# Kernel tuning notes

Hardware: AMD Instinct MI355X
Metric: run time of the kernel (lower is better)

## Reference

```python
import jax, jax.numpy as jnp
import numpy as np

N = 100000          # nodes
E = 3200000         # edges (avg degree 32)
F_IN = 128          # num_features
HID = 128           # hidden_channels
C = 8               # num_classes
G = 64              # graphs in batch
EPS = 1e-5


def setup_inputs() -> dict:
    key = jax.random.key(0)
    ks = jax.random.split(key, 10)
    x = jax.random.normal(ks[0], (N, F_IN), dtype=jnp.float32)
    edge_index = jax.random.randint(ks[1], (2, E), 0, N, dtype=jnp.int64)
    batch = jnp.sort(jax.random.randint(ks[2], (N,), 0, G, dtype=jnp.int64))
    # parameters
    glorot1 = float(np.sqrt(6.0 / (F_IN + HID)))
    W1 = jax.random.uniform(ks[3], (F_IN, HID), minval=-glorot1, maxval=glorot1, dtype=jnp.float32)
    conv1_bias = jnp.zeros((HID,), jnp.float32)
    bn_weight = jnp.ones((F_IN,), jnp.float32)
    bn_bias = jnp.zeros((F_IN,), jnp.float32)
    ln_weight = jnp.ones((HID,), jnp.float32)
    ln_bias = jnp.zeros((HID,), jnp.float32)
    glorot2 = float(np.sqrt(6.0 / (HID + C)))
    lin_W = jax.random.uniform(ks[4], (C, HID), minval=-glorot2, maxval=glorot2, dtype=jnp.float32)
    lin_b = jnp.zeros((C,), jnp.float32)
    return {"x": x, "edge_index": edge_index, "batch": batch,
            "bn_weight": bn_weight, "bn_bias": bn_bias,
            "W1": W1, "conv1_bias": conv1_bias,
            "ln_weight": ln_weight, "ln_bias": ln_bias,
            "lin_W": lin_W, "lin_b": lin_b}


def reference(x, edge_index, batch, bn_weight, bn_bias, W1, conv1_bias,
              ln_weight, ln_bias, lin_W, lin_b):
    n = x.shape[0]
    # BatchNorm1d over nodes (training-mode batch statistics, biased var)
    mu = x.mean(axis=0)
    var = x.var(axis=0)
    x = (x - mu) * jax.lax.rsqrt(var + EPS) * bn_weight + bn_bias
    # GCNConv: linear transform, add self-loops, symmetric normalization, scatter-add
    h = x @ W1                                   # [N, HID]
    loops = jnp.arange(n, dtype=edge_index.dtype)
    row = jnp.concatenate([edge_index[0], loops])  # source nodes
    col = jnp.concatenate([edge_index[1], loops])  # target nodes
    deg = jax.ops.segment_sum(jnp.ones_like(col, dtype=h.dtype), col, num_segments=N)
    dinv = jax.lax.rsqrt(deg)                    # deg >= 1 due to self-loops
    norm = dinv[row] * dinv[col]                 # [E+N]
    msg = h[row] * norm[:, None]                 # gather + scale
    h = jax.ops.segment_sum(msg, col, num_segments=N) + conv1_bias
    h = jax.nn.relu(h)
    # PyG LayerNorm, mode='graph', batch=None: normalize over the whole tensor
    h = h - h.mean()
    h = h * jax.lax.rsqrt(h.var() + EPS)
    h = h * ln_weight + ln_bias
    # global mean pool per graph
    counts = jax.ops.segment_sum(jnp.ones((n,), h.dtype), batch, num_segments=G)
    sums = jax.ops.segment_sum(h, batch, num_segments=G)
    g = sums / jnp.maximum(counts, 1.0)[:, None]  # [G, HID]
    return g @ lin_W.T + lin_b                    # [G, C]
```

## Files before the change

kernel.cpp:

```cpp
#include <hip/hip_runtime.h>

#define NN 100000
#define NE 3200000
#define F 128
#define NG 64
#define NC 8
#define EPSF 1e-5f

#define AGG_BLOCKS 25000
#define LDSTRIDE 136
#define BN_BLOCKS 1024

#define NBK 256
#define BNODES 391
#define BCAP 14336
#define CHUNK 4096
#define P1_BLOCKS ((NE + CHUNK - 1) / CHUNK)

typedef __attribute__((ext_vector_type(8))) short bf16x8;
typedef __attribute__((ext_vector_type(4))) float f32x4;
typedef _Float16 f16x2 __attribute__((ext_vector_type(2)));

union U32H2 { unsigned int u; f16x2 h; };
__device__ __forceinline__ f16x2 asH2(unsigned int u) { U32H2 c; c.u = u; return c.h; }
__device__ __forceinline__ unsigned int asU32(f16x2 h) { U32H2 c; c.h = h; return c.u; }

__device__ __forceinline__ unsigned short f2bf(float f) {
    unsigned int u = __float_as_uint(f);
    u = u + 0x7FFFu + ((u >> 16) & 1u);
    return (unsigned short)(u >> 16);
}
__device__ __forceinline__ unsigned short f2h_bits(float f) {
    union { _Float16 h; unsigned short u; } c;
    c.h = (_Float16)f;
    return c.u;
}

__global__ void bn_partial_k(const float* __restrict__ x, float* __restrict__ part,
                             int n, int rpb) {
    int tid = threadIdx.x, col = tid & 127, half = tid >> 7;
    int r0 = blockIdx.x * rpb, r1 = min(n, r0 + rpb);
    float s = 0.f, ss = 0.f;
    for (int r = r0 + half; r < r1; r += 2) {
        float v = x[(size_t)r * F + col];
        s += v; ss += v * v;
    }
    __shared__ float sh[512];
    sh[tid] = s; sh[256 + tid] = ss;
    __syncthreads();
    if (half == 0) {
        part[blockIdx.x * 256 + col]       = sh[col] + sh[col + 128];
        part[blockIdx.x * 256 + 128 + col] = sh[256 + col] + sh[256 + col + 128];
    }
}

__global__ void bn_finalize_k(const float* __restrict__ part,
                              const float* __restrict__ bnw, const float* __restrict__ bnb,
                              float* __restrict__ scale, float* __restrict__ shift, int n) {
    int col = blockIdx.x, tid = threadIdx.x;
    float s = 0.f, ss = 0.f;
    #pragma unroll
    for (int i = 0; i < 4; ++i) {
        int b = tid + i * 256;
        s  += part[b * 256 + col];
        ss += part[b * 256 + 128 + col];
    }
    __shared__ float shs[256], shss[256];
    shs[tid] = s; shss[tid] = ss;
    __syncthreads();
    for (int o = 128; o > 0; o >>= 1) {
        if (tid < o) { shs[tid] += shs[tid + o]; shss[tid] += shss[tid + o]; }
        __syncthreads();
    }
    if (tid == 0) {
        float mu  = shs[0] / (float)n;
        float var = shss[0] / (float)n - mu * mu;
        float rstd = rsqrtf(var + EPSF);
        float sc = bnw[col] * rstd;
        scale[col] = sc;
        shift[col] = bnb[col] - mu * sc;
    }
}

__global__ void prep_both_k(const float* __restrict__ W1, const float* __restrict__ scale,
                            const float* __restrict__ shift,
                            unsigned short* __restrict__ WpT, float* __restrict__ S) {
    int b = blockIdx.x, tid = threadIdx.x;
    if (b < 64) {
        int idx = b * 256 + tid;
        int k = idx >> 7, j = idx & 127;
        WpT[j * F + k] = f2bf(scale[k] * W1[idx]);
    } else {
        int j = b - 64;
        __shared__ float sh[256];
        sh[tid] = (tid < 128) ? shift[tid] * W1[tid * F + j] : 0.f;
        __syncthreads();
        for (int o = 128; o > 0; o >>= 1) {
            if (tid < o) sh[tid] += sh[tid + o];
            __syncthreads();
        }
        if (tid == 0) S[j] = sh[0];
    }
}

__global__ __launch_bounds__(256) void bucket_k(const int* __restrict__ ei,
                                                int* __restrict__ bcur,
                                                unsigned int* __restrict__ bbuf) {
    __shared__ int cntl[NBK];
    __shared__ int basel[NBK];
    __shared__ int gbase[NBK];
    __shared__ unsigned int ent[CHUNK];
    __shared__ unsigned char bid[CHUNK];
    int tid = threadIdx.x;
    int e0 = blockIdx.x * CHUNK;
    int ecnt = min(NE - e0, CHUNK);
    cntl[tid] = 0;
    __syncthreads();
    int myr[16], myc[16], myl[16];
    #pragma unroll
    for (int k = 0; k < 16; ++k) {
        int i = tid + k * 256;
        if (i < ecnt) {
            int r = ei[e0 + i];
            int c = ei[NE + e0 + i];
            myr[k] = r; myc[k] = c;
            myl[k] = atomicAdd(&cntl[(unsigned)c / BNODES], 1);
        } else { myr[k] = -1; myc[k] = 0; myl[k] = 0; }
    }
    __syncthreads();
    int myv = cntl[tid];
    basel[tid] = myv;
    __syncthreads();
    for (int o = 1; o < 256; o <<= 1) {
        int t = (tid >= o) ? basel[tid - o] : 0;
        __syncthreads();
        basel[tid] += t;
        __syncthreads();
    }
    basel[tid] -= myv;
    gbase[tid] = atomicAdd(&bcur[tid], myv);
    __syncthreads();
    #pragma unroll
    for (int k = 0; k < 16; ++k) {
        if (myr[k] >= 0) {
            int b = (unsigned)myc[k] / BNODES;
            int s = basel[b] + myl[k];
            ent[s] = ((unsigned)myr[k] << 9) | (unsigned)(myc[k] - b * BNODES);
            bid[s] = (unsigned char)b;
        }
    }
    __syncthreads();
    for (int s = tid; s < ecnt; s += 256) {
        unsigned int v = ent[s];
        int b = bid[s];
        int idx = s - basel[b] + gbase[b];
        if (idx < BCAP) bbuf[(size_t)b * BCAP + idx] = v;
    }
}

__global__ void bbase_k(const int* __restrict__ bcur, int* __restrict__ bbase,
                        int* __restrict__ offs) {
    int tid = threadIdx.x;
    __shared__ int s[256];
    int v = bcur[tid];
    s[tid] = v;
    __syncthreads();
    for (int o = 1; o < 256; o <<= 1) {
        int t = (tid >= o) ? s[tid - o] : 0;
        __syncthreads();
        s[tid] += t;
        __syncthreads();
    }
    bbase[tid] = s[tid] - v;
    if (tid == 255) offs[NN] = s[255];
}

__global__ void csr_k(const unsigned int* __restrict__ bbuf, const int* __restrict__ bcur,
                      const int* __restrict__ bbase,
                      int* __restrict__ offs, float* __restrict__ dinv,
                      int* __restrict__ srow) {
    int b = blockIdx.x, tid = threadIdx.x;
    __shared__ int h0[512], hA[512], hB[512];
    h0[tid] = 0; h0[tid + 256] = 0;
    __syncthreads();
    int m = min(bcur[b], BCAP);
    for (int i = tid; i < m; i += 256)
        atomicAdd(&h0[bbuf[(size_t)b * BCAP + i] & 511u], 1);
    __syncthreads();
    hA[tid] = h0[tid]; hA[tid + 256] = h0[tid + 256];
    __syncthreads();
    int* src = hA; int* dst = hB;
    for (int o = 1; o < 512; o <<= 1) {
        int i0 = tid, i1 = tid + 256;
        dst[i0] = src[i0] + ((i0 >= o) ? src[i0 - o] : 0);
        dst[i1] = src[i1] + ((i1 >= o) ? src[i1 - o] : 0);
        __syncthreads();
        int* tmp = src; src = dst; dst = tmp;
    }
    int nbase = b * BNODES;
    int base = bbase[b];
    int lim = min(BNODES, NN - nbase);
    for (int i = tid; i < lim; i += 256) {
        int d = h0[i];
        offs[nbase + i] = base + src[i] - d;
        dinv[nbase + i] = rsqrtf((float)d + 1.0f);
    }
    dst[tid] = src[tid] - h0[tid];
    dst[tid + 256] = src[tid + 256] - h0[tid + 256];
    __syncthreads();
    for (int i = tid; i < m; i += 256) {
        unsigned int v = bbuf[(size_t)b * BCAP + i];
        int dstl = (int)(v & 511u);
        int pos = base + atomicAdd(&dst[dstl], 1);
        srow[pos] = (int)(v >> 9);
    }
}

__global__ __launch_bounds__(256) void gemm_k(const float* __restrict__ x,
                                              const unsigned short* __restrict__ WpT,
                                              const float* __restrict__ S,
                                              const float* __restrict__ dinv,
                                              unsigned short* __restrict__ hf, int n) {
    __shared__ unsigned short wt[128 * LDSTRIDE];
    __shared__ unsigned short xt[64 * LDSTRIDE];
    int tid = threadIdx.x;
    int row0 = blockIdx.x * 64;
    for (int i = tid; i < 2048; i += 256) {
        int r = i >> 4, c = (i & 15) * 8;
        uint4 v = *(const uint4*)&WpT[r * F + c];
        *(uint4*)&wt[r * LDSTRIDE + c] = v;
    }
    for (int i = tid; i < 2048; i += 256) {
        int r = i >> 5, c = (i & 31) * 4;
        float4 v = make_float4(0.f, 0.f, 0.f, 0.f);
        if (row0 + r < n) v = *(const float4*)&x[(size_t)(row0 + r) * F + c];
        unsigned int p0 = (unsigned int)f2bf(v.x) | ((unsigned int)f2bf(v.y) << 16);
        unsigned int p1 = (unsigned int)f2bf(v.z) | ((unsigned int)f2bf(v.w) << 16);
        *(uint2*)&xt[r * LDSTRIDE + c] = make_uint2(p0, p1);
    }
    __syncthreads();
    int wv = tid >> 6, lane = tid & 63;
    int lm = lane & 15, lk = lane >> 4;
    bf16x8 afrag[4];
    #pragma unroll
    for (int kk = 0; kk < 4; ++kk)
        afrag[kk] = *(bf16x8*)&xt[(wv * 16 + lm) * LDSTRIDE + kk * 32 + lk * 8];
    float dv[4];
    #pragma unroll
    for (int j = 0; j < 4; ++j) {
        int r = row0 + wv * 16 + lk * 4 + j;
        dv[j] = (r < n) ? dinv[r] : 1.0f;
    }
    #pragma unroll
    for (int nt = 0; nt < 8; ++nt) {
        float sv = S[nt * 16 + lm];
        f32x4 acc = {sv, sv, sv, sv};
        #pragma unroll
        for (int kk = 0; kk < 4; ++kk) {
            bf16x8 b = *(bf16x8*)&wt[(nt * 16 + lm) * LDSTRIDE + kk * 32 + lk * 8];
            acc = __builtin_amdgcn_mfma_f32_16x16x32_bf16(afrag[kk], b, acc, 0, 0, 0);
        }
        #pragma unroll
        for (int j = 0; j < 4; ++j) {
            int r = row0 + wv * 16 + lk * 4 + j;
            if (r < n) hf[(size_t)r * F + nt * 16 + lm] = f2h_bits(acc[j] * dv[j]);
        }
    }
}

__global__ __launch_bounds__(256) void agg_k(const uint4* __restrict__ hb4,
                                             const int* __restrict__ srow,
                                             const int* __restrict__ offs,
                                             const float* __restrict__ dinv,
                                             const float* __restrict__ bias,
                                             uint4* __restrict__ h2p4,
                                             float* __restrict__ lnpart, int n) {
    int lane = threadIdx.x & 63, wv = threadIdx.x >> 6;
    int node = blockIdx.x * 4 + wv;
    int cg = lane & 15;
    int sub = lane >> 4;
    float s_part = 0.f, ss_part = 0.f;
    if (node < n) {
        int st = offs[node], en = offs[node + 1];
        float di = dinv[node];
        f16x2 a0 = {0.f16, 0.f16}, a1 = a0, a2 = a0, a3 = a0;
        if (sub == 0) {
            uint4 qs = hb4[(size_t)node * 16 + cg];
            a0 += asH2(qs.x); a1 += asH2(qs.y); a2 += asH2(qs.z); a3 += asH2(qs.w);
        }
        const uint4 qz = make_uint4(0u, 0u, 0u, 0u);
        for (int base = st; base < en; base += 64) {
            int m = en - base; if (m > 64) m = 64;
            int sv = (lane < m) ? srow[base + lane] : 0;
            int nq = (m + 3) >> 2;
            int k = 0;
            for (; k + 2 <= nq; k += 2) {
                int i0 = 4 * k + sub, i1 = i0 + 4;
                int sr0 = __shfl(sv, i0), sr1 = __shfl(sv, i1);
                bool v0 = i0 < m, v1 = i1 < m;
                uint4 q0 = hb4[(size_t)(v0 ? sr0 : node) * 16 + cg];
                uint4 q1 = hb4[(size_t)(v1 ? sr1 : node) * 16 + cg];
                if (!v0) q0 = qz;
                if (!v1) q1 = qz;
                a0 += asH2(q0.x); a1 += asH2(q0.y); a2 += asH2(q0.z); a3 += asH2(q0.w);
                a0 += asH2(q1.x); a1 += asH2(q1.y); a2 += asH2(q1.z); a3 += asH2(q1.w);
            }
            for (; k < nq; ++k) {
                int i0 = 4 * k + sub;
                int sr0 = __shfl(sv, i0);
                bool v0 = i0 < m;
                uint4 q0 = hb4[(size_t)(v0 ? sr0 : node) * 16 + cg];
                if (!v0) q0 = qz;
                a0 += asH2(q0.x); a1 += asH2(q0.y); a2 += asH2(q0.z); a3 += asH2(q0.w);
            }
        }
        a0 += asH2((unsigned int)__shfl_xor((int)asU32(a0), 16));
        a1 += asH2((unsigned int)__shfl_xor((int)asU32(a1), 16));
        a2 += asH2((unsigned int)__shfl_xor((int)asU32(a2), 16));
        a3 += asH2((unsigned int)__shfl_xor((int)asU32(a3), 16));
        a0 += asH2((unsigned int)__shfl_xor((int)asU32(a0), 32));
        a1 += asH2((unsigned int)__shfl_xor((int)asU32(a1), 32));
        a2 += asH2((unsigned int)__shfl_xor((int)asU32(a2), 32));
        a3 += asH2((unsigned int)__shfl_xor((int)asU32(a3), 32));
        float acc[8] = {(float)a0[0], (float)a0[1], (float)a1[0], (float)a1[1],
                        (float)a2[0], (float)a2[1], (float)a3[0], (float)a3[1]};
        float4 b0 = *(const float4*)&bias[cg * 8];
        float4 b1 = *(const float4*)&bias[cg * 8 + 4];
        float bv[8] = {b0.x, b0.y, b0.z, b0.w, b1.x, b1.y, b1.z, b1.w};
        float r[8];
        #pragma unroll
        for (int j = 0; j < 8; ++j) r[j] = fmaxf(fmaf(acc[j], di, bv[j]), 0.f);
        if (sub == 0) {
            uint4 p;
            p.x = asU32(f16x2{(_Float16)r[0], (_Float16)r[1]});
            p.y = asU32(f16x2{(_Float16)r[2], (_Float16)r[3]});
            p.z = asU32(f16x2{(_Float16)r[4], (_Float16)r[5]});
            p.w = asU32(f16x2{(_Float16)r[6], (_Float16)r[7]});
            h2p4[(size_t)node * 16 + cg] = p;
            #pragma unroll
            for (int j = 0; j < 8; ++j) {
                s_part += r[j];
                ss_part += r[j] * r[j];
            }
        }
    }
    __shared__ float sh[512];
    sh[threadIdx.x] = s_part; sh[256 + threadIdx.x] = ss_part;
    __syncthreads();
    for (int o = 128; o > 0; o >>= 1) {
        if (threadIdx.x < o) {
            sh[threadIdx.x] += sh[threadIdx.x + o];
            sh[256 + threadIdx.x] += sh[256 + threadIdx.x + o];
        }
        __syncthreads();
    }
    if (threadIdx.x == 0) {
        lnpart[blockIdx.x * 2]     = sh[0];
        lnpart[blockIdx.x * 2 + 1] = sh[256];
    }
}

__global__ void pool1_k(const unsigned int* __restrict__ h2p, const int* __restrict__ batch,
                        float* __restrict__ gsum, int n) {
    int tid = threadIdx.x, cp = tid & 63, half = tid >> 6;
    int n0 = blockIdx.x * 256, n1 = min(n, n0 + 256);
    int r = n0 + half;
    if (r >= n1) return;
    int gcur = batch[r];
    float a0 = 0.f, a1 = 0.f;
    for (; r < n1; r += 4) {
        int g = batch[r];
        f16x2 hp = asH2(h2p[(size_t)r * 64 + cp]);
        if (g != gcur) {
            atomicAdd(&gsum[gcur * F + cp * 2], a0);
            atomicAdd(&gsum[gcur * F + cp * 2 + 1], a1);
            a0 = a1 = 0.f; gcur = g;
        }
        a0 += (float)hp[0];
        a1 += (float)hp[1];
    }
    atomicAdd(&gsum[gcur * F + cp * 2], a0);
    atomicAdd(&gsum[gcur * F + cp * 2 + 1], a1);
}

__global__ void pool2_k(const float* __restrict__ gsum, const int* __restrict__ batch,
                        const float* __restrict__ lnpart, int nb,
                        const float* __restrict__ lnw, const float* __restrict__ lnb,
                        const float* __restrict__ linW, const float* __restrict__ linb,
                        float* __restrict__ out, int n) {
    int g = blockIdx.x, tid = threadIdx.x;
    __shared__ double shd[512];
    __shared__ float lnmu, lnrs;
    double s = 0.0, ss = 0.0;
    for (int i = tid; i < nb; i += 256) {
        s  += (double)lnpart[2 * i];
        ss += (double)lnpart[2 * i + 1];
    }
    shd[tid] = s; shd[256 + tid] = ss;
    __syncthreads();
    for (int o = 128; o > 0; o >>= 1) {
        if (tid < o) { shd[tid] += shd[tid + o]; shd[256 + tid] += shd[256 + tid + o]; }
        __syncthreads();
    }
    __shared__ int bounds[2];
    if (tid == 0) {
        double cnt = (double)NN * (double)F;
        double mu = shd[0] / cnt;
        double var = shd[256] / cnt - mu * mu;
        lnmu = (float)mu;
        lnrs = (float)(1.0 / sqrt(var + (double)EPSF));
    }
    if (tid < 2) {
        int target = g + tid;
        int lo = 0, hi = n;
        while (lo < hi) {
            int mid = (lo + hi) >> 1;
            if (batch[mid] < target) lo = mid + 1; else hi = mid;
        }
        bounds[tid] = lo;
    }
    __syncthreads();
    int cg = bounds[1] - bounds[0];
    __shared__ float vals[128];
    if (tid < 128) {
        float v = 0.f;
        if (cg > 0) {
            float m = gsum[g * F + tid] / (float)cg;
            v = (m - lnmu) * lnrs * lnw[tid] + lnb[tid];
        }
        vals[tid] = v;
    }
    __syncthreads();
    if (tid < NC) {
        float o = linb[tid];
        for (int k = 0; k < F; ++k) o = fmaf(vals[k], linW[tid * F + k], o);
        out[g * NC + tid] = o;
    }
}

extern "C" void kernel_launch(void* const* d_in, const int* in_sizes, int n_in,
                              void* d_out, int out_size, void* d_ws, size_t ws_size,
                              hipStream_t stream) {
    const float* x     = (const float*)d_in[0];
    const int*   ei    = (const int*)d_in[1];
    const int*   batch = (const int*)d_in[2];
    const float* bnw   = (const float*)d_in[3];
    const float* bnb   = (const float*)d_in[4];
    const float* W1    = (const float*)d_in[5];
    const float* cbias = (const float*)d_in[6];
    const float* lnw   = (const float*)d_in[7];
    const float* lnb   = (const float*)d_in[8];
    const float* linW  = (const float*)d_in[9];
    const float* linb  = (const float*)d_in[10];
    float* out = (float*)d_out;

    char* w = (char*)d_ws;
    size_t used = 0;
    auto alloc = [&](size_t bytes) {
        char* p = w;
        size_t pad = (bytes + 255) & ~(size_t)255;
        w += pad;
        used += pad;
        return p;
    };
    size_t bucket_bytes = (size_t)NBK * BCAP * 4;
    size_t hf_bytes     = (size_t)NN * F * 2;
    char* regionA = (char*)alloc(bucket_bytes > hf_bytes ? bucket_bytes : hf_bytes);
    unsigned int*   bbuf = (unsigned int*)regionA;
    unsigned short* hf   = (unsigned short*)regionA;

    unsigned int* h2p = (unsigned int*)alloc((size_t)NN * F * 2);
    int*   srow    = (int*)alloc((size_t)NE * 4);
    int*   offs    = (int*)alloc((size_t)(NN + 1) * 4);
    float* dinv    = (float*)alloc((size_t)NN * 4);
    int*   bcur    = (int*)alloc(NBK * 4);
    int*   bbase   = (int*)alloc(NBK * 4);
    float* bnpart  = (float*)alloc((size_t)BN_BLOCKS * 256 * 4);
    float* scale   = (float*)alloc(512);
    float* shift   = (float*)alloc(512);
    unsigned short* WpT = (unsigned short*)alloc(128 * 128 * 2);
    float* Svec    = (float*)alloc(512);
    float* lnpart  = (float*)alloc((size_t)AGG_BLOCKS * 2 * 4);
    float* gsum    = (float*)alloc((size_t)NG * F * 4);

    if (used > ws_size) {
        hipMemsetAsync(d_out, 0, (size_t)out_size * 4, stream);
        return;
    }

    hipMemsetAsync(bcur, 0, NBK * 4, stream);
    hipMemsetAsync(gsum, 0, (size_t)NG * F * 4, stream);

    int rpb = (NN + BN_BLOCKS - 1) / BN_BLOCKS;
    bn_partial_k<<<BN_BLOCKS, 256, 0, stream>>>(x, bnpart, NN, rpb);
    bn_finalize_k<<<128, 256, 0, stream>>>(bnpart, bnw, bnb, scale, shift, NN);
    prep_both_k<<<192, 256, 0, stream>>>(W1, scale, shift, WpT, Svec);

    bucket_k<<<P1_BLOCKS, 256, 0, stream>>>(ei, bcur, bbuf);
    bbase_k<<<1, 256, 0, stream>>>(bcur, bbase, offs);
    csr_k<<<NBK, 256, 0, stream>>>(bbuf, bcur, bbase, offs, dinv, srow);

    gemm_k<<<(NN + 63) / 64, 256, 0, stream>>>(x, WpT, Svec, dinv, hf, NN);
    agg_k<<<AGG_BLOCKS, 256, 0, stream>>>((const uint4*)hf, srow, offs, dinv,
                                          cbias, (uint4*)h2p, lnpart, NN);
    pool1_k<<<(NN + 255) / 256, 256, 0, stream>>>(h2p, batch, gsum, NN);
    pool2_k<<<NG, 256, 0, stream>>>(gsum, batch, lnpart, AGG_BLOCKS,
                                    lnw, lnb, linW, linb, out, NN);
}
```

Measured before the change: 285.5 us.

## Merge independent BN and CSR-build kernels into shared launches; unroll gather by four

Fuses the BatchNorm statistics kernels and the edge bucketing/CSR construction kernels pairwise into three combined launches, with block index ranges selecting the role. This lets the independent BN and graph-building stages run concurrently and cuts launch count from six to three. The aggregation inner loop is also unrolled from two to four gathers per iteration to put more loads in flight. The trade-offs are a larger combined shared-memory footprint per block, which may lower occupancy for the BN blocks, and higher register pressure in the aggregation kernel.

```diff
diff --git a/kernel.cpp b/kernel.cpp
--- a/kernel.cpp
+++ b/kernel.cpp
@@ -36,83 +36,35 @@
     return c.u;
 }
 
-__global__ void bn_partial_k(const float* __restrict__ x, float* __restrict__ part,
-                             int n, int rpb) {
-    int tid = threadIdx.x, col = tid & 127, half = tid >> 7;
-    int r0 = blockIdx.x * rpb, r1 = min(n, r0 + rpb);
-    float s = 0.f, ss = 0.f;
-    for (int r = r0 + half; r < r1; r += 2) {
-        float v = x[(size_t)r * F + col];
-        s += v; ss += v * v;
-    }
-    __shared__ float sh[512];
-    sh[tid] = s; sh[256 + tid] = ss;
-    __syncthreads();
-    if (half == 0) {
-        part[blockIdx.x * 256 + col]       = sh[col] + sh[col + 128];
-        part[blockIdx.x * 256 + 128 + col] = sh[256 + col] + sh[256 + col + 128];
-    }
-}
-
-__global__ void bn_finalize_k(const float* __restrict__ part,
-                              const float* __restrict__ bnw, const float* __restrict__ bnb,
-                              float* __restrict__ scale, float* __restrict__ shift, int n) {
-    int col = blockIdx.x, tid = threadIdx.x;
-    float s = 0.f, ss = 0.f;
-    #pragma unroll
-    for (int i = 0; i < 4; ++i) {
-        int b = tid + i * 256;
-        s  += part[b * 256 + col];
-        ss += part[b * 256 + 128 + col];
-    }
-    __shared__ float shs[256], shss[256];
-    shs[tid] = s; shss[tid] = ss;
-    __syncthreads();
-    for (int o = 128; o > 0; o >>= 1) {
-        if (tid < o) { shs[tid] += shs[tid + o]; shss[tid] += shss[tid + o]; }
-        __syncthreads();
-    }
-    if (tid == 0) {
-        float mu  = shs[0] / (float)n;
-        float var = shss[0] / (float)n - mu * mu;
-        float rstd = rsqrtf(var + EPSF);
-        float sc = bnw[col] * rstd;
-        scale[col] = sc;
-        shift[col] = bnb[col] - mu * sc;
-    }
-}
-
-__global__ void prep_both_k(const float* __restrict__ W1, const float* __restrict__ scale,
-                            const float* __restrict__ shift,
-                            unsigned short* __restrict__ WpT, float* __restrict__ S) {
-    int b = blockIdx.x, tid = threadIdx.x;
-    if (b < 64) {
-        int idx = b * 256 + tid;
-        int k = idx >> 7, j = idx & 127;
-        WpT[j * F + k] = f2bf(scale[k] * W1[idx]);
-    } else {
-        int j = b - 64;
-        __shared__ float sh[256];
-        sh[tid] = (tid < 128) ? shift[tid] * W1[tid * F + j] : 0.f;
-        __syncthreads();
-        for (int o = 128; o > 0; o >>= 1) {
-            if (tid < o) sh[tid] += sh[tid + o];
-            __syncthreads();
-        }
-        if (tid == 0) S[j] = sh[0];
-    }
-}
-
-__global__ __launch_bounds__(256) void bucket_k(const int* __restrict__ ei,
-                                                int* __restrict__ bcur,
-                                                unsigned int* __restrict__ bbuf) {
+__global__ __launch_bounds__(256) void bn_bucket_k(const float* __restrict__ x,
+                                                   float* __restrict__ part, int n, int rpb,
+                                                   const int* __restrict__ ei,
+                                                   int* __restrict__ bcur,
+                                                   unsigned int* __restrict__ bbuf) {
+    __shared__ float shf[512];
     __shared__ int cntl[NBK];
     __shared__ int basel[NBK];
     __shared__ int gbase[NBK];
     __shared__ unsigned int ent[CHUNK];
     __shared__ unsigned char bid[CHUNK];
     int tid = threadIdx.x;
-    int e0 = blockIdx.x * CHUNK;
+    if (blockIdx.x < BN_BLOCKS) {
+        int col = tid & 127, half = tid >> 7;
+        int r0 = blockIdx.x * rpb, r1 = min(n, r0 + rpb);
+        float s = 0.f, ss = 0.f;
+        for (int r = r0 + half; r < r1; r += 2) {
+            float v = x[(size_t)r * F + col];
+            s += v; ss += v * v;
+        }
+        shf[tid] = s; shf[256 + tid] = ss;
+        __syncthreads();
+        if (half == 0) {
+            part[blockIdx.x * 256 + col]       = shf[col] + shf[col + 128];
+            part[blockIdx.x * 256 + 128 + col] = shf[256 + col] + shf[256 + col + 128];
+        }
+        return;
+    }
+    int e0 = (blockIdx.x - BN_BLOCKS) * CHUNK;
     int ecnt = min(NE - e0, CHUNK);
     cntl[tid] = 0;
     __syncthreads();
@@ -158,9 +110,38 @@
     }
 }
 
-__global__ void bbase_k(const int* __restrict__ bcur, int* __restrict__ bbase,
-                        int* __restrict__ offs) {
+__global__ void finalize_both_k(const float* __restrict__ part,
+                                const float* __restrict__ bnw, const float* __restrict__ bnb,
+                                float* __restrict__ scale, float* __restrict__ shift, int n,
+                                const int* __restrict__ bcur, int* __restrict__ bbase,
+                                int* __restrict__ offs) {
     int tid = threadIdx.x;
+    if (blockIdx.x < 128) {
+        int col = blockIdx.x;
+        float s = 0.f, ss = 0.f;
+        #pragma unroll
+        for (int i = 0; i < 4; ++i) {
+            int b = tid + i * 256;
+            s  += part[b * 256 + col];
+            ss += part[b * 256 + 128 + col];
+        }
+        __shared__ float shs[256], shss[256];
+        shs[tid] = s; shss[tid] = ss;
+        __syncthreads();
+        for (int o = 128; o > 0; o >>= 1) {
+            if (tid < o) { shs[tid] += shs[tid + o]; shss[tid] += shss[tid + o]; }
+            __syncthreads();
+        }
+        if (tid == 0) {
+            float mu  = shs[0] / (float)n;
+            float var = shss[0] / (float)n - mu * mu;
+            float rstd = rsqrtf(var + EPSF);
+            float sc = bnw[col] * rstd;
+            scale[col] = sc;
+            shift[col] = bnb[col] - mu * sc;
+        }
+        return;
+    }
     __shared__ int s[256];
     int v = bcur[tid];
     s[tid] = v;
@@ -175,11 +156,33 @@
     if (tid == 255) offs[NN] = s[255];
 }
 
-__global__ void csr_k(const unsigned int* __restrict__ bbuf, const int* __restrict__ bcur,
-                      const int* __restrict__ bbase,
-                      int* __restrict__ offs, float* __restrict__ dinv,
-                      int* __restrict__ srow) {
-    int b = blockIdx.x, tid = threadIdx.x;
+__global__ void prep_csr_k(const float* __restrict__ W1, const float* __restrict__ scale,
+                           const float* __restrict__ shift,
+                           unsigned short* __restrict__ WpT, float* __restrict__ S,
+                           const unsigned int* __restrict__ bbuf, const int* __restrict__ bcur,
+                           const int* __restrict__ bbase,
+                           int* __restrict__ offs, float* __restrict__ dinv,
+                           int* __restrict__ srow) {
+    int tid = threadIdx.x;
+    if (blockIdx.x < 64) {
+        int idx = blockIdx.x * 256 + tid;
+        int k = idx >> 7, j = idx & 127;
+        WpT[j * F + k] = f2bf(scale[k] * W1[idx]);
+        return;
+    }
+    if (blockIdx.x < 192) {
+        int j = blockIdx.x - 64;
+        __shared__ float sh[256];
+        sh[tid] = (tid < 128) ? shift[tid] * W1[tid * F + j] : 0.f;
+        __syncthreads();
+        for (int o = 128; o > 0; o >>= 1) {
+            if (tid < o) sh[tid] += sh[tid + o];
+            __syncthreads();
+        }
+        if (tid == 0) S[j] = sh[0];
+        return;
+    }
+    int b = blockIdx.x - 192;
     __shared__ int h0[512], hA[512], hB[512];
     h0[tid] = 0; h0[tid + 256] = 0;
     __syncthreads();
@@ -294,16 +297,23 @@
             int sv = (lane < m) ? srow[base + lane] : 0;
             int nq = (m + 3) >> 2;
             int k = 0;
-            for (; k + 2 <= nq; k += 2) {
-                int i0 = 4 * k + sub, i1 = i0 + 4;
+            for (; k + 4 <= nq; k += 4) {
+                int i0 = 4 * k + sub, i1 = i0 + 4, i2 = i0 + 8, i3 = i0 + 12;
                 int sr0 = __shfl(sv, i0), sr1 = __shfl(sv, i1);
-                bool v0 = i0 < m, v1 = i1 < m;
+                int sr2 = __shfl(sv, i2), sr3 = __shfl(sv, i3);
+                bool v0 = i0 < m, v1 = i1 < m, v2 = i2 < m, v3 = i3 < m;
                 uint4 q0 = hb4[(size_t)(v0 ? sr0 : node) * 16 + cg];
                 uint4 q1 = hb4[(size_t)(v1 ? sr1 : node) * 16 + cg];
+                uint4 q2 = hb4[(size_t)(v2 ? sr2 : node) * 16 + cg];
+                uint4 q3 = hb4[(size_t)(v3 ? sr3 : node) * 16 + cg];
                 if (!v0) q0 = qz;
                 if (!v1) q1 = qz;
+                if (!v2) q2 = qz;
+                if (!v3) q3 = qz;
                 a0 += asH2(q0.x); a1 += asH2(q0.y); a2 += asH2(q0.z); a3 += asH2(q0.w);
                 a0 += asH2(q1.x); a1 += asH2(q1.y); a2 += asH2(q1.z); a3 += asH2(q1.w);
+                a0 += asH2(q2.x); a1 += asH2(q2.y); a2 += asH2(q2.z); a3 += asH2(q2.w);
+                a0 += asH2(q3.x); a1 += asH2(q3.y); a2 += asH2(q3.z); a3 += asH2(q3.w);
             }
             for (; k < nq; ++k) {
                 int i0 = 4 * k + sub;
@@ -492,13 +502,11 @@
     hipMemsetAsync(gsum, 0, (size_t)NG * F * 4, stream);
 
     int rpb = (NN + BN_BLOCKS - 1) / BN_BLOCKS;
-    bn_partial_k<<<BN_BLOCKS, 256, 0, stream>>>(x, bnpart, NN, rpb);
-    bn_finalize_k<<<128, 256, 0, stream>>>(bnpart, bnw, bnb, scale, shift, NN);
-    prep_both_k<<<192, 256, 0, stream>>>(W1, scale, shift, WpT, Svec);
-
-    bucket_k<<<P1_BLOCKS, 256, 0, stream>>>(ei, bcur, bbuf);
-    bbase_k<<<1, 256, 0, stream>>>(bcur, bbase, offs);
-    csr_k<<<NBK, 256, 0, stream>>>(bbuf, bcur, bbase, offs, dinv, srow);
+    bn_bucket_k<<<BN_BLOCKS + P1_BLOCKS, 256, 0, stream>>>(x, bnpart, NN, rpb, ei, bcur, bbuf);
+    finalize_both_k<<<129, 256, 0, stream>>>(bnpart, bnw, bnb, scale, shift, NN,
+                                             bcur, bbase, offs);
+    prep_csr_k<<<448, 256, 0, stream>>>(W1, scale, shift, WpT, Svec,
+                                        bbuf, bcur, bbase, offs, dinv, srow);
 
     gemm_k<<<(NN + 63) / 64, 256, 0, stream>>>(x, WpT, Svec, dinv, hf, NN);
     agg_k<<<AGG_BLOCKS, 256, 0, stream>>>((const uint4*)hf, srow, offs, dinv,
```

After: 267.7 us. 6.2% less time.
